# Optimization experiments

Measured on AMD Instinct MI355X. Metric: run time of the kernel, lower is better.

## Reference

```python
import jax, jax.numpy as jnp
import numpy as np

N = 25000        # nodes
E = 400000       # edges (avg degree 16)
F = 128          # num_features
NRBF = 20        # num_rbf_features
CUTOFF = 5.0


def setup_inputs() -> dict:
    key = jax.random.key(0)
    ks = jax.random.split(key, 9)
    node_scalar = jax.random.normal(ks[0], (N, F), jnp.float32)
    node_vector = jax.random.normal(ks[1], (N, F, 3), jnp.float32)
    dst = jax.random.randint(ks[2], (E,), 0, N)
    src = jax.random.randint(ks[3], (E,), 0, N)
    r = jax.random.normal(ks[4], (E, 3), jnp.float32) * 1.5
    d = jnp.clip(jnp.linalg.norm(r, axis=-1), 0.1, None)
    adj_matrix = jnp.concatenate(
        [dst[:, None].astype(jnp.float32), src[:, None].astype(jnp.float32), r, d[:, None]],
        axis=-1)  # [E, 6]
    s_in = 1.0 / np.sqrt(F)
    s_rbf = 1.0 / np.sqrt(NRBF)
    W1 = jax.random.normal(ks[5], (F, F), jnp.float32) * s_in
    b1 = jnp.zeros((F,), jnp.float32)
    W2 = jax.random.normal(ks[6], (F, 3 * F), jnp.float32) * s_in
    b2 = jnp.zeros((3 * F,), jnp.float32)
    Wr = jax.random.normal(ks[7], (NRBF, 3 * F), jnp.float32) * s_rbf
    br = jnp.zeros((3 * F,), jnp.float32)
    return dict(node_scalar=node_scalar, node_vector=node_vector, adj_matrix=adj_matrix,
                W1=W1, b1=b1, W2=W2, b2=b2, Wr=Wr, br=br)


def reference(node_scalar, node_vector, adj_matrix, W1, b1, W2, b2, Wr, br):
    # scalar message MLP: Linear -> SiLU -> Linear, [N, 3F]
    atom_scalar = jax.nn.silu(node_scalar @ W1 + b1) @ W2 + b2

    dst = adj_matrix[:, 0].astype(jnp.int32)
    src = adj_matrix[:, 1].astype(jnp.int32)
    r_ij = adj_matrix[:, 2:5]              # [E, 3]
    d = adj_matrix[:, 5]                   # [E]

    # sinc expansion: sin(d * n * pi / cutoff) / d, n = 1..NRBF -> [E, NRBF]
    n_vals = jnp.arange(1, NRBF + 1, dtype=jnp.float32)
    sinc = jnp.sin(d[:, None] * n_vals * jnp.pi / CUTOFF) / d[:, None]
    rbf = sinc @ Wr + br                   # [E, 3F]
    cut = jnp.where(d < CUTOFF, 0.5 * (jnp.cos(jnp.pi * d / CUTOFF) + 1.0), 0.0)
    w = rbf * cut[:, None]                 # [E, 3F]

    pre_split = atom_scalar[src] * w       # [E, 3F]
    s1, s2, s3 = jnp.split(pre_split, 3, axis=-1)  # each [E, F]

    r_hat = r_ij / d[:, None]              # [E, 3]
    # message_vector: [E, F, 3]
    message_vector = node_vector[src] * s1[:, :, None] + s3[:, :, None] * r_hat[:, None, :]

    delta_s = jnp.zeros_like(node_scalar).at[dst].add(s2)
    delta_v = jnp.zeros_like(node_vector).at[dst].add(message_vector)
    return node_scalar + delta_s, node_vector + delta_v
```

## Files before the change

### kernel.cpp

```cpp
#include <hip/hip_runtime.h>

#define FDIM 128
#define NRBF 20
constexpr float CUTOFF_F = 5.0f;
constexpr float PI_F = 3.14159265358979323846f;

typedef _Float16 h2 __attribute__((ext_vector_type(2)));
typedef _Float16 half4 __attribute__((ext_vector_type(4)));
typedef float f32x4 __attribute__((ext_vector_type(4)));

__device__ __forceinline__ uint packh(float a, float b) {
  union { _Float16 h[2]; uint u; } x;
  x.h[0] = (_Float16)a;
  x.h[1] = (_Float16)b;
  return x.u;
}
__device__ __forceinline__ float h_lo(uint w) {
  union { uint u; _Float16 h[2]; } x;
  x.u = w;
  return (float)x.h[0];
}
__device__ __forceinline__ float h_hi(uint w) {
  union { uint u; _Float16 h[2]; } x;
  x.u = w;
  return (float)x.h[1];
}
__device__ __forceinline__ float dot2(uint cw, h2 w, float acc) {
#if __has_builtin(__builtin_amdgcn_fdot2)
  h2 c = __builtin_bit_cast(h2, cw);
  return __builtin_amdgcn_fdot2(c, w, acc, false);
#else
  return fmaf(h_hi(cw), (float)w[1], fmaf(h_lo(cw), (float)w[0], acc));
#endif
}

struct Bun { uint x, y, z; };

__global__ __launch_bounds__(256) void wconv2(const float* __restrict__ W1,
                                              const float* __restrict__ W2,
                                              _Float16* __restrict__ w1h,
                                              _Float16* __restrict__ w2h,
                                              int* __restrict__ counts,
                                              int Ncnt) {
  int idx = blockIdx.x * blockDim.x + threadIdx.x;
  if (idx < Ncnt) counts[idx] = 0;
  const float* W;
  _Float16* outp;
  int NC, NCOLS, base;
  if (idx < 8 * 8 * 256) {
    W = W1; outp = w1h; NC = 8; NCOLS = 128; base = idx;
  } else if (idx < 8 * 8 * 256 + 8 * 24 * 256) {
    W = W2; outp = w2h; NC = 24; NCOLS = 384; base = idx - 8 * 8 * 256;
  } else {
    return;
  }
  int i = base & 3;
  int l = (base >> 2) & 63;
  int rem = base >> 8;
  int c = rem % NC, s = rem / NC;
  int k = s * 16 + ((l >> 4) & 3) * 4 + i;
  int col = c * 16 + (l & 15);
  outp[base] = (_Float16)W[(size_t)k * NCOLS + col];
}

__global__ __launch_bounds__(256) void gemm_fused(
    const float* __restrict__ A, const half4* __restrict__ w1h,
    const float* __restrict__ b1, const half4* __restrict__ w2h,
    const float* __restrict__ b2, const float* __restrict__ nvec,
    uint* __restrict__ bundle, int M) {
  __shared__ _Float16 Ah[64][136];
  const int t = threadIdx.x;
  const int w = t >> 6;
  const int l = t & 63;
  const int lr = l & 15, lg = (l >> 4) & 3;
  const int row0 = blockIdx.x * 64;

  for (int i = t; i < 64 * 32; i += 256) {
    int r = i >> 5, c4 = (i & 31) << 2;
    int gr = row0 + r;
    float4 v = make_float4(0.f, 0.f, 0.f, 0.f);
    if (gr < M) v = *(const float4*)&A[(size_t)gr * FDIM + c4];
    half4 hv = {(_Float16)v.x, (_Float16)v.y, (_Float16)v.z, (_Float16)v.w};
    *(half4*)&Ah[r][c4] = hv;
  }
  __syncthreads();

  half4 af[8];
#pragma unroll
  for (int s = 0; s < 8; ++s)
    af[s] = *(const half4*)&Ah[16 * w + lr][s * 16 + lg * 4];

  f32x4 acc1[8];
#pragma unroll
  for (int c = 0; c < 8; ++c) acc1[c] = {0.f, 0.f, 0.f, 0.f};
#pragma unroll
  for (int s = 0; s < 8; ++s) {
#pragma unroll
    for (int c = 0; c < 8; ++c) {
      half4 bf = w1h[(s * 8 + c) * 64 + l];
      acc1[c] = __builtin_amdgcn_mfma_f32_16x16x16f16(af[s], bf, acc1[c], 0, 0, 0);
    }
  }
  __syncthreads();
#pragma unroll
  for (int c = 0; c < 8; ++c) {
    float bb = b1[c * 16 + lr];
#pragma unroll
    for (int r = 0; r < 4; ++r) {
      float x = acc1[c][r] + bb;
      x = x / (1.f + __expf(-x));
      Ah[16 * w + lg * 4 + r][c * 16 + lr] = (_Float16)x;
    }
  }
  __syncthreads();

  half4 hf[8];
#pragma unroll
  for (int s = 0; s < 8; ++s)
    hf[s] = *(const half4*)&Ah[16 * w + lr][s * 16 + lg * 4];

#pragma unroll 1
  for (int cg = 0; cg < 8; ++cg) {
    f32x4 a3[3];
#pragma unroll
    for (int p = 0; p < 3; ++p) a3[p] = {0.f, 0.f, 0.f, 0.f};
#pragma unroll
    for (int s = 0; s < 8; ++s) {
#pragma unroll
      for (int p = 0; p < 3; ++p) {
        half4 bf = w2h[(s * 24 + cg + p * 8) * 64 + l];
        a3[p] = __builtin_amdgcn_mfma_f32_16x16x16f16(hf[s], bf, a3[p], 0, 0, 0);
      }
    }
    const int j = cg * 16 + lr;
    const float bb0 = b2[j], bb1 = b2[j + 128], bb2 = b2[j + 256];
#pragma unroll
    for (int r = 0; r < 4; ++r) {
      int n = row0 + 16 * w + lg * 4 + r;
      if (n >= M) continue;
      const float* vb = nvec + ((size_t)n * FDIM + j) * 3;
      float v0 = vb[0], v1 = vb[1], v2 = vb[2];
      uint* o = bundle + ((size_t)n * FDIM + j) * 3;
      o[0] = packh(a3[0][r] + bb0, a3[1][r] + bb1);
      o[1] = packh(a3[2][r] + bb2, v0);
      o[2] = packh(v1, v2);
    }
  }
}

__global__ __launch_bounds__(256) void hist_kernel(const float* __restrict__ adj,
                                                   int* __restrict__ counts,
                                                   int E) {
  int e = blockIdx.x * blockDim.x + threadIdx.x;
  if (e < E) atomicAdd(&counts[(int)adj[(size_t)e * 6]], 1);
}

__global__ __launch_bounds__(1024) void scan_kernel(
    const int* __restrict__ counts, int* __restrict__ offs,
    int* __restrict__ cursor, int n) {
  __shared__ int part[1024];
  const int tid = threadIdx.x;
  const int CH = (n + 1023) >> 10;
  const int b = tid * CH;
  const int e = min(b + CH, n);
  int s = 0;
  for (int i = b; i < e; ++i) s += counts[i];
  part[tid] = s;
  __syncthreads();
  for (int off = 1; off < 1024; off <<= 1) {
    int v = (tid >= off) ? part[tid - off] : 0;
    __syncthreads();
    part[tid] += v;
    __syncthreads();
  }
  int run = part[tid] - s;
  if (tid == 0) offs[0] = 0;
  for (int i = b; i < e; ++i) {
    int c = counts[i];
    cursor[i] = run;
    run += c;
    offs[i + 1] = run;
  }
}

__global__ __launch_bounds__(256) void edge_prep(const float* __restrict__ adj,
                                                 int* __restrict__ cursor,
                                                 int* __restrict__ eids,
                                                 uint* __restrict__ rec, int E) {
  int e = blockIdx.x * blockDim.x + threadIdx.x;
  if (e >= E) return;
  const float* a = adj + (size_t)e * 6;
  int dst = (int)a[0];
  int src = (int)a[1];
  float rx = a[2], ry = a[3], rz = a[4], d = a[5];

  int p = atomicAdd(&cursor[dst], 1);
  eids[p] = e;

  float x = d * (PI_F / CUTOFF_F);
  float sx, cx;
  __sincosf(x, &sx, &cx);
  float invd = 1.f / d;
  float cut = (d < CUTOFF_F) ? 0.5f * (cx + 1.f) : 0.f;
  float sc = invd * cut;

  union { uint w[14]; uint2 q[7]; } R;
  R.w[0] = (uint)src;
  R.w[1] = packh(rx * invd, ry * invd);
  R.w[2] = packh(rz * invd, cut);
  float twoc = 2.f * cx;
  float sprev = 0.f, scur = sx;
  float c[NRBF];
#pragma unroll
  for (int n = 0; n < NRBF; ++n) {
    c[n] = scur * sc;
    float nxt = fmaf(twoc, scur, -sprev);
    sprev = scur;
    scur = nxt;
  }
#pragma unroll
  for (int m = 0; m < 10; ++m) R.w[3 + m] = packh(c[2 * m], c[2 * m + 1]);
  R.w[13] = 0;
  uint2* o = (uint2*)(rec + (size_t)p * 14);
#pragma unroll
  for (int m = 0; m < 7; ++m) o[m] = R.q[m];
}

__global__ __launch_bounds__(128) void accum_kernel(
    const uint* __restrict__ rec, const uint* __restrict__ bundle,
    const float* __restrict__ nvec, const float* __restrict__ Wr,
    const float* __restrict__ br, const float* __restrict__ ns,
    const int* __restrict__ offs, const int* __restrict__ eids,
    float* __restrict__ out_s, float* __restrict__ out_v, int Nn) {
  const int j = threadIdx.x;

  h2 wp0[10], wp1[10], wp2[10];
#pragma unroll
  for (int m = 0; m < 10; ++m) {
    wp0[m] = h2{(_Float16)Wr[(2 * m) * 384 + j], (_Float16)Wr[(2 * m + 1) * 384 + j]};
    wp1[m] = h2{(_Float16)Wr[(2 * m) * 384 + 128 + j], (_Float16)Wr[(2 * m + 1) * 384 + 128 + j]};
    wp2[m] = h2{(_Float16)Wr[(2 * m) * 384 + 256 + j], (_Float16)Wr[(2 * m + 1) * 384 + 256 + j]};
  }
  const float brj0 = br[j], brj1 = br[j + 128], brj2 = br[j + 256];

  __shared__ int sh_e[128], sh_pos[128], sh_src[128];

#define LOADREC(R, t)                                                      \
  {                                                                        \
    int su = __builtin_amdgcn_readfirstlane(beg + sh_pos[(t)]);            \
    const uint* p = rec + (size_t)(uint)su * 14;                           \
    _Pragma("unroll") for (int w_ = 0; w_ < 13; ++w_) R[w_] = p[w_];       \
  }
#define LOADB(B, tt)                                                       \
  {                                                                        \
    int su = __builtin_amdgcn_readfirstlane(sh_src[(tt)]);                 \
    const uint* p = bundle + ((size_t)(uint)su * FDIM + j) * 3;            \
    (B).x = p[0];                                                          \
    (B).y = p[1];                                                          \
    (B).z = p[2];                                                          \
  }
#define COMPUTE(RC, BB)                                                    \
  {                                                                        \
    float rhx = h_lo(RC[1]), rhy = h_hi(RC[1]);                            \
    float rhz = h_lo(RC[2]), cut = h_hi(RC[2]);                            \
    float w0 = cut * brj0, w1 = cut * brj1, w2 = cut * brj2;               \
    _Pragma("unroll") for (int q = 0; q < 10; ++q) {                       \
      w0 = dot2(RC[3 + q], wp0[q], w0);                                    \
      w1 = dot2(RC[3 + q], wp1[q], w1);                                    \
      w2 = dot2(RC[3 + q], wp2[q], w2);                                    \
    }                                                                      \
    float s1 = h_lo((BB).x) * w0;                                          \
    float s2 = h_hi((BB).x) * w1;                                          \
    float s3 = h_lo((BB).y) * w2;                                          \
    float pv0 = h_hi((BB).y), pv1 = h_lo((BB).z), pv2 = h_hi((BB).z);      \
    acc_s += s2;                                                           \
    av0 = fmaf(pv0, s1, fmaf(s3, rhx, av0));                               \
    av1 = fmaf(pv1, s1, fmaf(s3, rhy, av1));                               \
    av2 = fmaf(pv2, s1, fmaf(s3, rhz, av2));                               \
  }

  for (int d = blockIdx.x; d < Nn; d += gridDim.x) {
    const int beg = offs[d];
    const int cnt = offs[d + 1] - beg;
    const int m = cnt < 128 ? cnt : 128;
    if (j < m) sh_e[j] = eids[beg + j];
    __syncthreads();
    if (j < m) {
      int v = sh_e[j];
      int r = 0;
      for (int u = 0; u < m; ++u) r += (sh_e[u] < v);
      sh_pos[r] = j;
      sh_src[r] = (int)rec[(size_t)(uint)(beg + j) * 14];
    }
    __syncthreads();

    float acc_s = 0.f, av0 = 0.f, av1 = 0.f, av2 = 0.f;

    uint r_cur[13], r_nxt[13];
    Bun b0_ = {}, b1_ = {}, b2_ = {}, b3_ = {};
    if (m > 0) { LOADB(b0_, 0); LOADREC(r_cur, 0); }
    if (m > 1) { LOADB(b1_, 1); LOADREC(r_nxt, 1); }
    if (m > 2) LOADB(b2_, 2);

    for (int t = 0; t < m; ++t) {
      if (t + 3 < m) LOADB(b3_, t + 3);
      uint r_n2[13];
      if (t + 2 < m) LOADREC(r_n2, t + 2);

      COMPUTE(r_cur, b0_);

#pragma unroll
      for (int w_ = 0; w_ < 13; ++w_) {
        r_cur[w_] = r_nxt[w_];
        r_nxt[w_] = r_n2[w_];
      }
      b0_ = b1_;
      b1_ = b2_;
      b2_ = b3_;
    }

    for (int t = 128; t < cnt; ++t) {
      uint R[13];
      {
        int su = __builtin_amdgcn_readfirstlane(beg + t);
        const uint* p = rec + (size_t)(uint)su * 14;
#pragma unroll
        for (int w_ = 0; w_ < 13; ++w_) R[w_] = p[w_];
      }
      Bun Bx;
      {
        const uint* p = bundle + ((size_t)(uint)R[0] * FDIM + j) * 3;
        Bx.x = p[0];
        Bx.y = p[1];
        Bx.z = p[2];
      }
      COMPUTE(R, Bx);
    }

    out_s[(size_t)d * FDIM + j] = ns[(size_t)d * FDIM + j] + acc_s;
    float* vo = out_v + (size_t)d * 384 + j * 3;
    const float* vi = nvec + (size_t)d * 384 + j * 3;
    vo[0] = vi[0] + av0;
    vo[1] = vi[1] + av1;
    vo[2] = vi[2] + av2;
  }
#undef LOADREC
#undef LOADB
#undef COMPUTE
}

extern "C" void kernel_launch(void* const* d_in, const int* in_sizes, int n_in,
                              void* d_out, int out_size, void* d_ws,
                              size_t ws_size, hipStream_t stream) {
  const float* node_scalar = (const float*)d_in[0];
  const float* node_vector = (const float*)d_in[1];
  const float* adj = (const float*)d_in[2];
  const float* W1 = (const float*)d_in[3];
  const float* b1 = (const float*)d_in[4];
  const float* W2 = (const float*)d_in[5];
  const float* b2 = (const float*)d_in[6];
  const float* Wr = (const float*)d_in[7];
  const float* br = (const float*)d_in[8];

  const int N = in_sizes[0] / FDIM;
  const int E = in_sizes[2] / 6;

  float* out = (float*)d_out;
  float* out_s = out;
  float* out_v = out + (size_t)N * FDIM;

  char* w = (char*)d_ws;
  uint* bundle = (uint*)w;
  size_t off = (size_t)N * FDIM * 12;
  uint* rec = (uint*)(w + off);
  off += (size_t)E * 56;
  _Float16* w1h = (_Float16*)(w + off);
  off += 8 * 8 * 256 * 2;
  _Float16* w2h = (_Float16*)(w + off);
  off += 8 * 24 * 256 * 2;
  int* counts = (int*)(w + off);
  int* offs = counts + N;
  int* cursor = offs + N + 1;
  int* eids = cursor + N;

  wconv2<<<(8 * 8 * 256 + 8 * 24 * 256 + 255) / 256, 256, 0, stream>>>(
      W1, W2, w1h, w2h, counts, N);
  hist_kernel<<<(E + 255) / 256, 256, 0, stream>>>(adj, counts, E);
  scan_kernel<<<1, 1024, 0, stream>>>(counts, offs, cursor, N);
  edge_prep<<<(E + 255) / 256, 256, 0, stream>>>(adj, cursor, eids, rec, E);

  gemm_fused<<<(N + 63) / 64, 256, 0, stream>>>(node_scalar, (const half4*)w1h,
                                                b1, (const half4*)w2h, b2,
                                                node_vector, bundle, N);

  const int agrid = N < 4096 ? N : 4096;
  accum_kernel<<<agrid, 128, 0, stream>>>(rec, bundle, node_vector, Wr, br,
                                          node_scalar, offs, eids, out_s,
                                          out_v, N);
}
```

Before: 320.4 us.

## Merge edge prep and node GEMM into one launch; restructure accum prefetch

The separate edge_prep and gemm_fused kernels become one launch. Block indices select either the node GEMM path or the per-edge preprocessing path, so the two independent stages can overlap and one launch is saved. In accum_kernel the shared-memory src table is removed: each bundle load now takes its src index from the already-loaded record word. The loop becomes a three-way rotating buffer instead of register shifting. This drops one extra gather per edge and the register copies, but makes each bundle load depend on its record load, which shortens the prefetch distance.

Result: faster. 303.2 us (-5.4%).

```diff
diff --git a/kernel.cpp b/kernel.cpp
--- a/kernel.cpp
+++ b/kernel.cpp
@@ -63,91 +63,6 @@
   outp[base] = (_Float16)W[(size_t)k * NCOLS + col];
 }
 
-__global__ __launch_bounds__(256) void gemm_fused(
-    const float* __restrict__ A, const half4* __restrict__ w1h,
-    const float* __restrict__ b1, const half4* __restrict__ w2h,
-    const float* __restrict__ b2, const float* __restrict__ nvec,
-    uint* __restrict__ bundle, int M) {
-  __shared__ _Float16 Ah[64][136];
-  const int t = threadIdx.x;
-  const int w = t >> 6;
-  const int l = t & 63;
-  const int lr = l & 15, lg = (l >> 4) & 3;
-  const int row0 = blockIdx.x * 64;
-
-  for (int i = t; i < 64 * 32; i += 256) {
-    int r = i >> 5, c4 = (i & 31) << 2;
-    int gr = row0 + r;
-    float4 v = make_float4(0.f, 0.f, 0.f, 0.f);
-    if (gr < M) v = *(const float4*)&A[(size_t)gr * FDIM + c4];
-    half4 hv = {(_Float16)v.x, (_Float16)v.y, (_Float16)v.z, (_Float16)v.w};
-    *(half4*)&Ah[r][c4] = hv;
-  }
-  __syncthreads();
-
-  half4 af[8];
-#pragma unroll
-  for (int s = 0; s < 8; ++s)
-    af[s] = *(const half4*)&Ah[16 * w + lr][s * 16 + lg * 4];
-
-  f32x4 acc1[8];
-#pragma unroll
-  for (int c = 0; c < 8; ++c) acc1[c] = {0.f, 0.f, 0.f, 0.f};
-#pragma unroll
-  for (int s = 0; s < 8; ++s) {
-#pragma unroll
-    for (int c = 0; c < 8; ++c) {
-      half4 bf = w1h[(s * 8 + c) * 64 + l];
-      acc1[c] = __builtin_amdgcn_mfma_f32_16x16x16f16(af[s], bf, acc1[c], 0, 0, 0);
-    }
-  }
-  __syncthreads();
-#pragma unroll
-  for (int c = 0; c < 8; ++c) {
-    float bb = b1[c * 16 + lr];
-#pragma unroll
-    for (int r = 0; r < 4; ++r) {
-      float x = acc1[c][r] + bb;
-      x = x / (1.f + __expf(-x));
-      Ah[16 * w + lg * 4 + r][c * 16 + lr] = (_Float16)x;
-    }
-  }
-  __syncthreads();
-
-  half4 hf[8];
-#pragma unroll
-  for (int s = 0; s < 8; ++s)
-    hf[s] = *(const half4*)&Ah[16 * w + lr][s * 16 + lg * 4];
-
-#pragma unroll 1
-  for (int cg = 0; cg < 8; ++cg) {
-    f32x4 a3[3];
-#pragma unroll
-    for (int p = 0; p < 3; ++p) a3[p] = {0.f, 0.f, 0.f, 0.f};
-#pragma unroll
-    for (int s = 0; s < 8; ++s) {
-#pragma unroll
-      for (int p = 0; p < 3; ++p) {
-        half4 bf = w2h[(s * 24 + cg + p * 8) * 64 + l];
-        a3[p] = __builtin_amdgcn_mfma_f32_16x16x16f16(hf[s], bf, a3[p], 0, 0, 0);
-      }
-    }
-    const int j = cg * 16 + lr;
-    const float bb0 = b2[j], bb1 = b2[j + 128], bb2 = b2[j + 256];
-#pragma unroll
-    for (int r = 0; r < 4; ++r) {
-      int n = row0 + 16 * w + lg * 4 + r;
-      if (n >= M) continue;
-      const float* vb = nvec + ((size_t)n * FDIM + j) * 3;
-      float v0 = vb[0], v1 = vb[1], v2 = vb[2];
-      uint* o = bundle + ((size_t)n * FDIM + j) * 3;
-      o[0] = packh(a3[0][r] + bb0, a3[1][r] + bb1);
-      o[1] = packh(a3[2][r] + bb2, v0);
-      o[2] = packh(v1, v2);
-    }
-  }
-}
-
 __global__ __launch_bounds__(256) void hist_kernel(const float* __restrict__ adj,
                                                    int* __restrict__ counts,
                                                    int E) {
@@ -183,47 +98,133 @@
   }
 }
 
-__global__ __launch_bounds__(256) void edge_prep(const float* __restrict__ adj,
-                                                 int* __restrict__ cursor,
-                                                 int* __restrict__ eids,
-                                                 uint* __restrict__ rec, int E) {
-  int e = blockIdx.x * blockDim.x + threadIdx.x;
-  if (e >= E) return;
-  const float* a = adj + (size_t)e * 6;
-  int dst = (int)a[0];
-  int src = (int)a[1];
-  float rx = a[2], ry = a[3], rz = a[4], d = a[5];
-
-  int p = atomicAdd(&cursor[dst], 1);
-  eids[p] = e;
-
-  float x = d * (PI_F / CUTOFF_F);
-  float sx, cx;
-  __sincosf(x, &sx, &cx);
-  float invd = 1.f / d;
-  float cut = (d < CUTOFF_F) ? 0.5f * (cx + 1.f) : 0.f;
-  float sc = invd * cut;
-
-  union { uint w[14]; uint2 q[7]; } R;
-  R.w[0] = (uint)src;
-  R.w[1] = packh(rx * invd, ry * invd);
-  R.w[2] = packh(rz * invd, cut);
-  float twoc = 2.f * cx;
-  float sprev = 0.f, scur = sx;
-  float c[NRBF];
-#pragma unroll
-  for (int n = 0; n < NRBF; ++n) {
-    c[n] = scur * sc;
-    float nxt = fmaf(twoc, scur, -sprev);
-    sprev = scur;
-    scur = nxt;
-  }
-#pragma unroll
-  for (int m = 0; m < 10; ++m) R.w[3 + m] = packh(c[2 * m], c[2 * m + 1]);
-  R.w[13] = 0;
-  uint2* o = (uint2*)(rec + (size_t)p * 14);
-#pragma unroll
-  for (int m = 0; m < 7; ++m) o[m] = R.q[m];
+__global__ __launch_bounds__(256) void prep_gemm(
+    const float* __restrict__ A, const half4* __restrict__ w1h,
+    const float* __restrict__ b1, const half4* __restrict__ w2h,
+    const float* __restrict__ b2, const float* __restrict__ nvec,
+    uint* __restrict__ bundle, int M, const float* __restrict__ adj,
+    int* __restrict__ cursor, int* __restrict__ eids, uint* __restrict__ rec,
+    int E, int GB) {
+  __shared__ _Float16 Ah[64][136];
+  const int t = threadIdx.x;
+
+  if ((int)blockIdx.x >= GB) {
+    int e = ((int)blockIdx.x - GB) * 256 + t;
+    if (e >= E) return;
+    const float* a = adj + (size_t)e * 6;
+    int dst = (int)a[0];
+    int src = (int)a[1];
+    float rx = a[2], ry = a[3], rz = a[4], d = a[5];
+
+    int p = atomicAdd(&cursor[dst], 1);
+    eids[p] = e;
+
+    float x = d * (PI_F / CUTOFF_F);
+    float sx, cx;
+    __sincosf(x, &sx, &cx);
+    float invd = 1.f / d;
+    float cut = (d < CUTOFF_F) ? 0.5f * (cx + 1.f) : 0.f;
+    float sc = invd * cut;
+
+    union { uint w[14]; uint2 q[7]; } R;
+    R.w[0] = (uint)src;
+    R.w[1] = packh(rx * invd, ry * invd);
+    R.w[2] = packh(rz * invd, cut);
+    float twoc = 2.f * cx;
+    float sprev = 0.f, scur = sx;
+    float c[NRBF];
+#pragma unroll
+    for (int n = 0; n < NRBF; ++n) {
+      c[n] = scur * sc;
+      float nxt = fmaf(twoc, scur, -sprev);
+      sprev = scur;
+      scur = nxt;
+    }
+#pragma unroll
+    for (int m = 0; m < 10; ++m) R.w[3 + m] = packh(c[2 * m], c[2 * m + 1]);
+    R.w[13] = 0;
+    uint2* o = (uint2*)(rec + (size_t)p * 14);
+#pragma unroll
+    for (int m = 0; m < 7; ++m) o[m] = R.q[m];
+    return;
+  }
+
+  const int w = t >> 6;
+  const int l = t & 63;
+  const int lr = l & 15, lg = (l >> 4) & 3;
+  const int row0 = blockIdx.x * 64;
+
+  for (int i = t; i < 64 * 32; i += 256) {
+    int r = i >> 5, c4 = (i & 31) << 2;
+    int gr = row0 + r;
+    float4 v = make_float4(0.f, 0.f, 0.f, 0.f);
+    if (gr < M) v = *(const float4*)&A[(size_t)gr * FDIM + c4];
+    half4 hv = {(_Float16)v.x, (_Float16)v.y, (_Float16)v.z, (_Float16)v.w};
+    *(half4*)&Ah[r][c4] = hv;
+  }
+  __syncthreads();
+
+  half4 af[8];
+#pragma unroll
+  for (int s = 0; s < 8; ++s)
+    af[s] = *(const half4*)&Ah[16 * w + lr][s * 16 + lg * 4];
+
+  f32x4 acc1[8];
+#pragma unroll
+  for (int c = 0; c < 8; ++c) acc1[c] = {0.f, 0.f, 0.f, 0.f};
+#pragma unroll
+  for (int s = 0; s < 8; ++s) {
+#pragma unroll
+    for (int c = 0; c < 8; ++c) {
+      half4 bf = w1h[(s * 8 + c) * 64 + l];
+      acc1[c] = __builtin_amdgcn_mfma_f32_16x16x16f16(af[s], bf, acc1[c], 0, 0, 0);
+    }
+  }
+  __syncthreads();
+#pragma unroll
+  for (int c = 0; c < 8; ++c) {
+    float bb = b1[c * 16 + lr];
+#pragma unroll
+    for (int r = 0; r < 4; ++r) {
+      float x = acc1[c][r] + bb;
+      x = x / (1.f + __expf(-x));
+      Ah[16 * w + lg * 4 + r][c * 16 + lr] = (_Float16)x;
+    }
+  }
+  __syncthreads();
+
+  half4 hf[8];
+#pragma unroll
+  for (int s = 0; s < 8; ++s)
+    hf[s] = *(const half4*)&Ah[16 * w + lr][s * 16 + lg * 4];
+
+#pragma unroll 1
+  for (int cg = 0; cg < 8; ++cg) {
+    f32x4 a3[3];
+#pragma unroll
+    for (int p = 0; p < 3; ++p) a3[p] = {0.f, 0.f, 0.f, 0.f};
+#pragma unroll
+    for (int s = 0; s < 8; ++s) {
+#pragma unroll
+      for (int p = 0; p < 3; ++p) {
+        half4 bf = w2h[(s * 24 + cg + p * 8) * 64 + l];
+        a3[p] = __builtin_amdgcn_mfma_f32_16x16x16f16(hf[s], bf, a3[p], 0, 0, 0);
+      }
+    }
+    const int j = cg * 16 + lr;
+    const float bb0 = b2[j], bb1 = b2[j + 128], bb2 = b2[j + 256];
+#pragma unroll
+    for (int r = 0; r < 4; ++r) {
+      int n = row0 + 16 * w + lg * 4 + r;
+      if (n >= M) continue;
+      const float* vb = nvec + ((size_t)n * FDIM + j) * 3;
+      float v0 = vb[0], v1 = vb[1], v2 = vb[2];
+      uint* o = bundle + ((size_t)n * FDIM + j) * 3;
+      o[0] = packh(a3[0][r] + bb0, a3[1][r] + bb1);
+      o[1] = packh(a3[2][r] + bb2, v0);
+      o[2] = packh(v1, v2);
+    }
+  }
 }
 
 __global__ __launch_bounds__(128) void accum_kernel(
@@ -243,18 +244,18 @@
   }
   const float brj0 = br[j], brj1 = br[j + 128], brj2 = br[j + 256];
 
-  __shared__ int sh_e[128], sh_pos[128], sh_src[128];
-
+  __shared__ int sh_e[128], sh_pos[128];
+
+#define SLOT(t) ((t) < 128 ? sh_pos[(t)] : (t))
 #define LOADREC(R, t)                                                      \
   {                                                                        \
-    int su = __builtin_amdgcn_readfirstlane(beg + sh_pos[(t)]);            \
+    int su = __builtin_amdgcn_readfirstlane(beg + SLOT(t));                \
     const uint* p = rec + (size_t)(uint)su * 14;                           \
     _Pragma("unroll") for (int w_ = 0; w_ < 13; ++w_) R[w_] = p[w_];       \
   }
-#define LOADB(B, tt)                                                       \
+#define LOADB(B, SRC)                                                      \
   {                                                                        \
-    int su = __builtin_amdgcn_readfirstlane(sh_src[(tt)]);                 \
-    const uint* p = bundle + ((size_t)(uint)su * FDIM + j) * 3;            \
+    const uint* p = bundle + ((size_t)(uint)(SRC)*FDIM + j) * 3;           \
     (B).x = p[0];                                                          \
     (B).y = p[1];                                                          \
     (B).z = p[2];                                                          \
@@ -290,33 +291,30 @@
       int r = 0;
       for (int u = 0; u < m; ++u) r += (sh_e[u] < v);
       sh_pos[r] = j;
-      sh_src[r] = (int)rec[(size_t)(uint)(beg + j) * 14];
     }
     __syncthreads();
 
     float acc_s = 0.f, av0 = 0.f, av1 = 0.f, av2 = 0.f;
 
-    uint r_cur[13], r_nxt[13];
-    Bun b0_ = {}, b1_ = {}, b2_ = {}, b3_ = {};
-    if (m > 0) { LOADB(b0_, 0); LOADREC(r_cur, 0); }
-    if (m > 1) { LOADB(b1_, 1); LOADREC(r_nxt, 1); }
-    if (m > 2) LOADB(b2_, 2);
-
-    for (int t = 0; t < m; ++t) {
-      if (t + 3 < m) LOADB(b3_, t + 3);
-      uint r_n2[13];
-      if (t + 2 < m) LOADREC(r_n2, t + 2);
-
-      COMPUTE(r_cur, b0_);
-
-#pragma unroll
-      for (int w_ = 0; w_ < 13; ++w_) {
-        r_cur[w_] = r_nxt[w_];
-        r_nxt[w_] = r_n2[w_];
-      }
-      b0_ = b1_;
-      b1_ = b2_;
-      b2_ = b3_;
+    uint r0[13], r1[13], r2[13];
+    Bun b0_ = {}, b1_ = {}, b2_ = {};
+    if (m > 0) LOADREC(r0, 0);
+    if (m > 1) LOADREC(r1, 1);
+    if (m > 0) LOADB(b0_, r0[0]);
+    if (m > 1) LOADB(b1_, r1[0]);
+
+    for (int t = 0; t < m; t += 3) {
+      if (t + 2 < m) LOADREC(r2, t + 2);
+      COMPUTE(r0, b0_);
+      if (t + 2 < m) LOADB(b2_, r2[0]);
+      if (t + 1 >= m) break;
+      if (t + 3 < m) LOADREC(r0, t + 3);
+      COMPUTE(r1, b1_);
+      if (t + 3 < m) LOADB(b0_, r0[0]);
+      if (t + 2 >= m) break;
+      if (t + 4 < m) LOADREC(r1, t + 4);
+      COMPUTE(r2, b2_);
+      if (t + 4 < m) LOADB(b1_, r1[0]);
     }
 
     for (int t = 128; t < cnt; ++t) {
@@ -328,12 +326,7 @@
         for (int w_ = 0; w_ < 13; ++w_) R[w_] = p[w_];
       }
       Bun Bx;
-      {
-        const uint* p = bundle + ((size_t)(uint)R[0] * FDIM + j) * 3;
-        Bx.x = p[0];
-        Bx.y = p[1];
-        Bx.z = p[2];
-      }
+      LOADB(Bx, R[0]);
       COMPUTE(R, Bx);
     }
 
@@ -344,6 +337,7 @@
     vo[1] = vi[1] + av1;
     vo[2] = vi[2] + av2;
   }
+#undef SLOT
 #undef LOADREC
 #undef LOADB
 #undef COMPUTE
@@ -387,11 +381,13 @@
       W1, W2, w1h, w2h, counts, N);
   hist_kernel<<<(E + 255) / 256, 256, 0, stream>>>(adj, counts, E);
   scan_kernel<<<1, 1024, 0, stream>>>(counts, offs, cursor, N);
-  edge_prep<<<(E + 255) / 256, 256, 0, stream>>>(adj, cursor, eids, rec, E);
-
-  gemm_fused<<<(N + 63) / 64, 256, 0, stream>>>(node_scalar, (const half4*)w1h,
-                                                b1, (const half4*)w2h, b2,
-                                                node_vector, bundle, N);
+
+  const int GB = (N + 63) / 64;
+  const int EB = (E + 255) / 256;
+  prep_gemm<<<GB + EB, 256, 0, stream>>>(node_scalar, (const half4*)w1h, b1,
+                                         (const half4*)w2h, b2, node_vector,
+                                         bundle, N, adj, cursor, eids, rec, E,
+                                         GB);
 
   const int agrid = N < 4096 ? N : 4096;
   accum_kernel<<<agrid, 128, 0, stream>>>(rec, bundle, node_vector, Wr, br,
```
